# Performance work log

Hardware: AMD Instinct MI355X
Metric: run time of the kernel (lower is better)

## Reference

```python
import jax, jax.numpy as jnp
import numpy as np
import math

H, SQK, SV, PQK, PV = 12, 16, 16, 4, 8
C1, C2 = 384, 128
B, N = 1, 768


def _rand_rot(key, shape):
    # random proper rotation matrices via QR of gaussian matrices
    m = jax.random.normal(key, shape + (3, 3), dtype=jnp.float32)
    q, r = jnp.linalg.qr(m)
    d = jnp.sign(jnp.diagonal(r, axis1=-2, axis2=-1))
    return q * d[..., None, :]


def setup_inputs() -> dict:
    key = jax.random.key(0)
    ks = jax.random.split(key, 16)
    s = 0.05
    return {
        'act': jax.random.normal(ks[0], (B, N, C1), dtype=jnp.float32),
        'act_2d': jax.random.normal(ks[1], (B, N, N, C2), dtype=jnp.float32),
        'sequence_mask': jnp.ones((B, N, 1), dtype=jnp.float32),
        'rot': _rand_rot(ks[2], (B, N)),
        'trans': jax.random.normal(ks[3], (B, N, 3), dtype=jnp.float32),
        'wq': jax.random.normal(ks[4], (C1, H * SQK), dtype=jnp.float32) * s,
        'wk': jax.random.normal(ks[5], (C1, H * SQK), dtype=jnp.float32) * s,
        'wv': jax.random.normal(ks[6], (C1, H * SV), dtype=jnp.float32) * s,
        'wqp': jax.random.normal(ks[7], (C1, H * PQK * 3), dtype=jnp.float32) * s,
        'bqp': jnp.zeros((H * PQK * 3,), dtype=jnp.float32),
        'wkp': jax.random.normal(ks[8], (C1, H * PQK * 3), dtype=jnp.float32) * s,
        'bkp': jnp.zeros((H * PQK * 3,), dtype=jnp.float32),
        'wvp': jax.random.normal(ks[9], (C1, H * PV * 3), dtype=jnp.float32) * s,
        'bvp': jnp.zeros((H * PV * 3,), dtype=jnp.float32),
        'w2d': jax.random.normal(ks[10], (C2, H), dtype=jnp.float32) * s,
        'b2d': jnp.zeros((H,), dtype=jnp.float32),
        'wfin': jax.random.normal(ks[11], (H * (C2 + SV + 4 * PV), C1), dtype=jnp.float32) * s,
        'bfin': jnp.zeros((C1,), dtype=jnp.float32),
        'tw': jnp.zeros((H,), dtype=jnp.float32),
    }


def _points(act, w, b, P):
    # torch: view [...,H,P*3] -> split into 3 chunks of P -> stack last => layout [H,3,P]
    p = (act @ w + b).reshape(*act.shape[:-1], H, 3, P)
    p = jnp.moveaxis(p, -2, -1)  # [B,N,H,P,3]
    return p.reshape(*act.shape[:-1], H * P, 3)


def _ipa(act, act_2d, sequence_mask, rot, trans,
         wq, wk, wv, wqp, bqp, wkp, bkp, wvp, bvp, w2d, b2d, wfin, bfin, tw):
    b, n, _ = act.shape
    q = (act @ wq).reshape(b, n, H, SQK) * math.sqrt(1.0 / SQK)
    k = (act @ wk).reshape(b, n, H, SQK)
    v = (act @ wv).reshape(b, n, H, SV)

    apply = lambda p: jnp.einsum('bnij,bnpj->bnpi', rot, p) + trans[:, :, None, :]
    qp = apply(_points(act, wqp, bqp, PQK))  # [B,N,H*PQK,3]
    kp = apply(_points(act, wkp, bkp, PQK))
    vp = apply(_points(act, wvp, bvp, PV))   # [B,N,H*PV,3]

    # point-distance logits
    pw = math.sqrt(2.0 / (9.0 * PQK)) * jax.nn.softplus(tw)  # [H]
    d2 = jnp.sum(jnp.square(qp[:, :, None] - kp[:, None]), -1)  # [B,N,N,H*PQK]
    d2 = d2.reshape(b, n, n, H, PQK).sum(-1)                    # [B,N,N,H]
    logits = -0.5 * pw * d2
    logits = logits + jnp.einsum('bqhc,bkhc->bqkh', q, k)
    logits = logits + act_2d @ w2d + b2d
    mask_2d = sequence_mask * jnp.swapaxes(sequence_mask, -1, -2)  # [B,N,N]
    logits = logits - 1e5 * (1.0 - mask_2d)[..., None]
    logits = logits * math.sqrt(1.0 / 3.0)
    attn = jax.nn.softmax(logits, axis=-2)  # over key residues

    res_scalar = jnp.einsum('bqkh,bkhc->bqhc', attn, v).reshape(b, n, H * SV)
    vp5 = vp.reshape(b, n, H, PV, 3)
    rpg = jnp.einsum('bqkh,bkhpd->bqhpd', attn, vp5).reshape(b, n, H * PV, 3)
    rpl = jnp.einsum('bnji,bnpj->bnpi', rot, rpg - trans[:, :, None, :])  # invert_apply
    norms = jnp.linalg.norm(rpl, axis=-1)
    r2d = jnp.einsum('bijh,bijc->bihc', attn, act_2d).reshape(b, n, H * C2)
    final = jnp.concatenate(
        [res_scalar, rpl[..., 0], rpl[..., 1], rpl[..., 2], norms, r2d], axis=-1)
    return final @ wfin + bfin


def reference(act, act_2d, sequence_mask, rot, trans,
              wq, wk, wv, wqp, bqp, wkp, bkp, wvp, bvp, w2d, b2d, wfin, bfin, tw):
    return _ipa(act, act_2d, sequence_mask, rot, trans,
                wq, wk, wv, wqp, bqp, wkp, bkp, wvp, bvp, w2d, b2d, wfin, bfin, tw)
```

## Files before the change

### kernel.cpp

```cpp
#include <hip/hip_runtime.h>
#include <math.h>

#define NH    12
#define NRES  768
#define C1V   384
#define C2V   128
#define NPROJ 1152
#define QKD   28
#define FDIM  2112
#define VVD   480
#define APAD  772
#define KSPLIT 11

__device__ __forceinline__ float softplusf_(float x) {
    return (x > 20.f) ? x : log1pf(__expf(x));
}

__global__ __launch_bounds__(256) void k1_proj(
    const float* __restrict__ act,
    const float* __restrict__ wq, const float* __restrict__ wk,
    const float* __restrict__ wv, const float* __restrict__ wqp,
    const float* __restrict__ wkp, const float* __restrict__ wvp,
    const float* __restrict__ bqp, const float* __restrict__ bkp,
    const float* __restrict__ bvp, float* __restrict__ proj)
{
    __shared__ float As[64 * 33];
    __shared__ float Bs[32 * 65];
    const int n0 = blockIdx.x * 64, m0 = blockIdx.y * 64;
    const int tid = threadIdx.x;
    const int tx = tid & 15, ty = tid >> 4;
    float c[4][4] = {};

    for (int kt = 0; kt < C1V; kt += 32) {
        for (int idx = tid; idx < 64 * 32; idx += 256) {
            int r = idx >> 5, j = idx & 31;
            As[r * 33 + j] = act[(m0 + r) * C1V + kt + j];
        }
        for (int idx = tid; idx < 32 * 64; idx += 256) {
            int r = idx >> 6, col = idx & 63;
            int jj = n0 + col, k = kt + r;
            float w;
            if      (jj < 192) w = wq [k * 192 + jj];
            else if (jj < 384) w = wk [k * 192 + jj - 192];
            else if (jj < 576) w = wv [k * 192 + jj - 384];
            else if (jj < 720) w = wqp[k * 144 + jj - 576];
            else if (jj < 864) w = wkp[k * 144 + jj - 720];
            else               w = wvp[k * 288 + jj - 864];
            Bs[r * 65 + col] = w;
        }
        __syncthreads();
        #pragma unroll
        for (int kk = 0; kk < 32; ++kk) {
            float a[4], b[4];
            #pragma unroll
            for (int i = 0; i < 4; ++i) a[i] = As[(ty * 4 + i) * 33 + kk];
            #pragma unroll
            for (int j = 0; j < 4; ++j) b[j] = Bs[kk * 65 + tx * 4 + j];
            #pragma unroll
            for (int i = 0; i < 4; ++i)
                #pragma unroll
                for (int j = 0; j < 4; ++j) c[i][j] += a[i] * b[j];
        }
        __syncthreads();
    }
    float biasv[4];
    #pragma unroll
    for (int j = 0; j < 4; ++j) {
        int col = n0 + tx * 4 + j;
        biasv[j] = (col >= 864) ? bvp[col - 864]
                 : (col >= 720) ? bkp[col - 720]
                 : (col >= 576) ? bqp[col - 576] : 0.f;
    }
    #pragma unroll
    for (int i = 0; i < 4; ++i) {
        float4 v;
        v.x = c[i][0] + biasv[0]; v.y = c[i][1] + biasv[1];
        v.z = c[i][2] + biasv[2]; v.w = c[i][3] + biasv[3];
        *(float4*)&proj[(m0 + ty * 4 + i) * NPROJ + n0 + tx * 4] = v;
    }
}

__global__ __launch_bounds__(64) void k2_prep(
    const float* __restrict__ proj, const float* __restrict__ rot,
    const float* __restrict__ trans, const float* __restrict__ tw,
    float* __restrict__ Qv, float* __restrict__ Kv,
    float* __restrict__ akArr, float* __restrict__ vv)
{
    const int n = blockIdx.x, tid = threadIdx.x;
    __shared__ float kp2[48];
    const float* pr = proj + n * NPROJ;
    float R[9], T[3];
    #pragma unroll
    for (int i = 0; i < 9; ++i) R[i] = rot[n * 9 + i];
    #pragma unroll
    for (int i = 0; i < 3; ++i) T[i] = trans[n * 3 + i];

    for (int idx = tid; idx < 192; idx += 64) {
        int h = idx >> 4, cc = idx & 15;
        Qv[(n * NH + h) * QKD + cc] = pr[idx] * 0.25f;
        Kv[(n * NH + h) * QKD + cc] = pr[192 + idx];
        vv[n * VVD + idx] = pr[384 + idx];
    }
    if (tid < 48) {
        int h = tid >> 2, p = tid & 3;
        float pwh = 0.23570226039551584f * softplusf_(tw[h]);
        float lx = pr[576 + h * 12 + p];
        float ly = pr[576 + h * 12 + 4 + p];
        float lz = pr[576 + h * 12 + 8 + p];
        float gx = R[0] * lx + R[1] * ly + R[2] * lz + T[0];
        float gy = R[3] * lx + R[4] * ly + R[5] * lz + T[1];
        float gz = R[6] * lx + R[7] * ly + R[8] * lz + T[2];
        float* qd = &Qv[(n * NH + h) * QKD + 16];
        qd[p] = pwh * gx; qd[4 + p] = pwh * gy; qd[8 + p] = pwh * gz;
        lx = pr[720 + h * 12 + p];
        ly = pr[720 + h * 12 + 4 + p];
        lz = pr[720 + h * 12 + 8 + p];
        gx = R[0] * lx + R[1] * ly + R[2] * lz + T[0];
        gy = R[3] * lx + R[4] * ly + R[5] * lz + T[1];
        gz = R[6] * lx + R[7] * ly + R[8] * lz + T[2];
        float* kd = &Kv[(n * NH + h) * QKD + 16];
        kd[p] = gx; kd[4 + p] = gy; kd[8 + p] = gz;
        kp2[tid] = gx * gx + gy * gy + gz * gz;
    }
    __syncthreads();
    if (tid < NH) {
        float pwh = 0.23570226039551584f * softplusf_(tw[tid]);
        akArr[n * NH + tid] = -0.5f * pwh *
            (kp2[tid * 4] + kp2[tid * 4 + 1] + kp2[tid * 4 + 2] + kp2[tid * 4 + 3]);
    }
    for (int idx = tid; idx < 96; idx += 64) {
        int h = idx >> 3, p = idx & 7;
        float lx = pr[864 + h * 24 + p];
        float ly = pr[864 + h * 24 + 8 + p];
        float lz = pr[864 + h * 24 + 16 + p];
        float gx = R[0] * lx + R[1] * ly + R[2] * lz + T[0];
        float gy = R[3] * lx + R[4] * ly + R[5] * lz + T[1];
        float gz = R[6] * lx + R[7] * ly + R[8] * lz + T[2];
        float* dst = &vv[n * VVD + 192 + h * 24 + p * 3];
        dst[0] = gx; dst[1] = gy; dst[2] = gz;
    }
}

__global__ __launch_bounds__(256) void k2b_qk(
    const float* __restrict__ Qv, const float* __restrict__ Kv,
    const float* __restrict__ akArr, float* __restrict__ qkBuf)
{
    const int h = blockIdx.z;
    const int k0 = blockIdx.x * 64, q0 = blockIdx.y * 64;
    __shared__ float As[64 * 29];
    __shared__ float Bs[64 * 29];
    const int tid = threadIdx.x, tx = tid & 15, ty = tid >> 4;

    for (int idx = tid; idx < 64 * 28; idx += 256) {
        int r = idx / 28, j = idx - r * 28;
        As[r * 29 + j] = Qv[((q0 + r) * NH + h) * QKD + j];
        Bs[r * 29 + j] = Kv[((k0 + r) * NH + h) * QKD + j];
    }
    __syncthreads();
    float c[4][4] = {};
    #pragma unroll
    for (int kk = 0; kk < 28; ++kk) {
        float a[4], b[4];
        #pragma unroll
        for (int i = 0; i < 4; ++i) a[i] = As[(ty * 4 + i) * 29 + kk];
        #pragma unroll
        for (int j = 0; j < 4; ++j) b[j] = Bs[(tx * 4 + j) * 29 + kk];
        #pragma unroll
        for (int i = 0; i < 4; ++i)
            #pragma unroll
            for (int j = 0; j < 4; ++j) c[i][j] += a[i] * b[j];
    }
    float akv[4];
    #pragma unroll
    for (int j = 0; j < 4; ++j) akv[j] = akArr[(k0 + tx * 4 + j) * NH + h];
    #pragma unroll
    for (int i = 0; i < 4; ++i) {
        float4 v;
        v.x = c[i][0] + akv[0]; v.y = c[i][1] + akv[1];
        v.z = c[i][2] + akv[2]; v.w = c[i][3] + akv[3];
        *(float4*)&qkBuf[((q0 + ty * 4 + i) * NH + h) * NRES + k0 + tx * 4] = v;
    }
}

__global__ __launch_bounds__(256) void kA_bias(
    const float* __restrict__ act2d, const float* __restrict__ smask,
    const float* __restrict__ w2d, float* __restrict__ qkBuf)
{
    const int q = blockIdx.y, k0 = blockIdx.x * 64, tid = threadIdx.x;
    __shared__ float tile[64 * 129];
    __shared__ float w2dS[NH * 128];

    for (int idx = tid; idx < C2V * NH; idx += 256)
        w2dS[(idx % NH) * 128 + (idx / NH)] = w2d[idx];
    const float* src = act2d + ((size_t)q * NRES + k0) * C2V;
    #pragma unroll
    for (int i = 0; i < 8; ++i) {
        int f = tid + i * 256;
        float4 v = ((const float4*)src)[f];
        int r = f >> 5, cq = f & 31;
        float* dst = &tile[r * 129 + cq * 4];
        dst[0] = v.x; dst[1] = v.y; dst[2] = v.z; dst[3] = v.w;
    }
    __syncthreads();

    const int r = tid & 63, g = tid >> 6;
    const float* trow = &tile[r * 129];
    const float* w0 = &w2dS[(3 * g    ) * 128];
    const float* w1 = &w2dS[(3 * g + 1) * 128];
    const float* w2 = &w2dS[(3 * g + 2) * 128];
    float d0 = 0.f, d1 = 0.f, d2 = 0.f;
    #pragma unroll
    for (int c = 0; c < 128; ++c) {
        float t = trow[c];
        d0 += t * w0[c];
        d1 += t * w1[c];
        d2 += t * w2[c];
    }
    const int k = k0 + r;
    const float msk = -1e5f * (1.f - smask[q] * smask[k]);
    const float scale = 0.5773502691896258f;
    size_t i0 = ((size_t)(q * NH + 3 * g    )) * NRES + k;
    size_t i1 = ((size_t)(q * NH + 3 * g + 1)) * NRES + k;
    size_t i2 = ((size_t)(q * NH + 3 * g + 2)) * NRES + k;
    qkBuf[i0] = (qkBuf[i0] + d0 + msk) * scale;
    qkBuf[i1] = (qkBuf[i1] + d1 + msk) * scale;
    qkBuf[i2] = (qkBuf[i2] + d2 + msk) * scale;
}

__global__ __launch_bounds__(256) void kC_attn(
    const float* __restrict__ act2d, const float* __restrict__ qkBuf,
    const float* __restrict__ vv, const float* __restrict__ rot,
    const float* __restrict__ trans, float* __restrict__ F)
{
    const int q = blockIdx.x, tid = threadIdx.x;
    __shared__ float attnS[NH * APAD];
    __shared__ float tile[24 * 128];
    __shared__ float red[NH * 4];
    __shared__ float mh[NH], lh[NH];
    __shared__ float rotS[9], transS[3];

    if (tid < 9) rotS[tid] = rot[q * 9 + tid];
    if (tid < 3) transS[tid] = trans[q * 3 + tid];

    float lg[3][NH];
    #pragma unroll
    for (int h = 0; h < NH; ++h)
        #pragma unroll
        for (int i = 0; i < 3; ++i)
            lg[i][h] = qkBuf[((size_t)(q * NH + h)) * NRES + tid + 256 * i];

    const int wv_ = tid >> 6, lane = tid & 63;
    #pragma unroll
    for (int h = 0; h < NH; ++h) {
        float v = fmaxf(fmaxf(lg[0][h], lg[1][h]), lg[2][h]);
        for (int off = 32; off > 0; off >>= 1) v = fmaxf(v, __shfl_down(v, off, 64));
        if (lane == 0) red[h * 4 + wv_] = v;
    }
    __syncthreads();
    if (tid < NH)
        mh[tid] = fmaxf(fmaxf(red[tid * 4], red[tid * 4 + 1]),
                        fmaxf(red[tid * 4 + 2], red[tid * 4 + 3]));
    __syncthreads();
    float lsum[NH];
    #pragma unroll
    for (int h = 0; h < NH; ++h) lsum[h] = 0.f;
    #pragma unroll
    for (int i = 0; i < 3; ++i)
        #pragma unroll
        for (int h = 0; h < NH; ++h) {
            float e = __expf(lg[i][h] - mh[h]);
            attnS[h * APAD + tid + 256 * i] = e;
            lsum[h] += e;
        }
    #pragma unroll
    for (int h = 0; h < NH; ++h) {
        float v = lsum[h];
        for (int off = 32; off > 0; off >>= 1) v += __shfl_down(v, off, 64);
        if (lane == 0) red[h * 4 + wv_] = v;
    }
    __syncthreads();
    if (tid < NH)
        lh[tid] = 1.f / (red[tid * 4] + red[tid * 4 + 1] + red[tid * 4 + 2] + red[tid * 4 + 3]);

    const int c = tid & 127, kg = tid >> 7;
    float acc[NH];
    #pragma unroll
    for (int h = 0; h < NH; ++h) acc[h] = 0.f;

    for (int s = 0; s < 32; ++s) {
        const int k0 = s * 24;
        __syncthreads();
        const float* src = act2d + ((size_t)q * NRES + k0) * C2V;
        #pragma unroll
        for (int i = 0; i < 3; ++i) {
            int f = tid + i * 256;
            ((float4*)tile)[f] = ((const float4*)src)[f];
        }
        __syncthreads();
        #pragma unroll
        for (int k4 = 0; k4 < 3; ++k4) {
            const int kb = kg * 12 + k4 * 4;
            float4 av[NH];
            #pragma unroll
            for (int h = 0; h < NH; ++h)
                av[h] = *(const float4*)&attnS[h * APAD + k0 + kb];
            #pragma unroll
            for (int u = 0; u < 4; ++u) {
                float t = tile[(kb + u) * 128 + c];
                #pragma unroll
                for (int h = 0; h < NH; ++h)
                    acc[h] += ((const float*)&av[h])[u] * t;
            }
        }
    }
    __syncthreads();
    if (kg == 1) {
        #pragma unroll
        for (int h = 0; h < NH; ++h) tile[h * 128 + c] = acc[h];
    }
    __syncthreads();
    float* Fq = F + q * FDIM;
    if (kg == 0) {
        #pragma unroll
        for (int h = 0; h < NH; ++h)
            Fq[576 + h * 128 + c] = (acc[h] + tile[h * 128 + c]) * lh[h];
    }
    __syncthreads();

    const int j4 = tid & 127;
    const int kgv = tid >> 7;
    float p0 = 0.f, p1 = 0.f, p2 = 0.f, p3 = 0.f;
    if (j4 < 120) {
        const int h = (j4 < 48) ? (j4 >> 2) : ((j4 - 48) / 6);
        const float* at = &attnS[h * APAD + kgv * 384];
        const float* col = vv + (size_t)(kgv * 384) * VVD + j4 * 4;
        #pragma unroll 4
        for (int k = 0; k < 384; ++k) {
            float a = at[k];
            float4 v = *(const float4*)(col + (size_t)k * VVD);
            p0 += a * v.x; p1 += a * v.y; p2 += a * v.z; p3 += a * v.w;
        }
    }
    __syncthreads();
    if (j4 < 120) {
        float4 pv = {p0, p1, p2, p3};
        *(float4*)&tile[(kgv * 120 + j4) * 4] = pv;
    }
    __syncthreads();
    if (tid < 120) {
        float4 a = *(const float4*)&tile[tid * 4];
        float4 b = *(const float4*)&tile[(120 + tid) * 4];
        const int h = (tid < 48) ? (tid >> 2) : ((tid - 48) / 6);
        const float il = lh[h];
        float4 s = {(a.x + b.x) * il, (a.y + b.y) * il,
                    (a.z + b.z) * il, (a.w + b.w) * il};
        if (tid < 48) {
            *(float4*)&Fq[tid * 4] = s;
        } else {
            *(float4*)&tile[1024 + (tid - 48) * 4] = s;
        }
    }
    __syncthreads();
    if (tid < 96) {
        float gx = tile[1024 + tid * 3]     - transS[0];
        float gy = tile[1024 + tid * 3 + 1] - transS[1];
        float gz = tile[1024 + tid * 3 + 2] - transS[2];
        float x = rotS[0] * gx + rotS[3] * gy + rotS[6] * gz;
        float y = rotS[1] * gx + rotS[4] * gy + rotS[7] * gz;
        float z = rotS[2] * gx + rotS[5] * gy + rotS[8] * gz;
        Fq[192 + tid] = x;
        Fq[288 + tid] = y;
        Fq[384 + tid] = z;
        Fq[480 + tid] = sqrtf(x * x + y * y + z * z);
    }
}

__global__ __launch_bounds__(256) void k5_partial(
    const float* __restrict__ F, const float* __restrict__ wfin,
    float* __restrict__ part)
{
    const int n0 = blockIdx.x * 64, m0 = blockIdx.y * 64, kz = blockIdx.z;
    const int kbeg = kz * 192;
    __shared__ float As[64 * 33];
    __shared__ float Bs[32 * 65];
    const int tid = threadIdx.x, tx = tid & 15, ty = tid >> 4;
    float c[4][4] = {};

    for (int kt = kbeg; kt < kbeg + 192; kt += 32) {
        for (int idx = tid; idx < 64 * 32; idx += 256) {
            int r = idx >> 5, j = idx & 31;
            As[r * 33 + j] = F[(m0 + r) * FDIM + kt + j];
        }
        for (int idx = tid; idx < 32 * 64; idx += 256) {
            int r = idx >> 6, col = idx & 63;
            Bs[r * 65 + col] = wfin[(kt + r) * 384 + n0 + col];
        }
        __syncthreads();
        #pragma unroll
        for (int kk = 0; kk < 32; ++kk) {
            float a[4], b[4];
            #pragma unroll
            for (int i = 0; i < 4; ++i) a[i] = As[(ty * 4 + i) * 33 + kk];
            #pragma unroll
            for (int j = 0; j < 4; ++j) b[j] = Bs[kk * 65 + tx * 4 + j];
            #pragma unroll
            for (int i = 0; i < 4; ++i)
                #pragma unroll
                for (int j = 0; j < 4; ++j) c[i][j] += a[i] * b[j];
        }
        __syncthreads();
    }
    float* dst = part + (size_t)kz * (768 * 384);
    #pragma unroll
    for (int i = 0; i < 4; ++i) {
        float4 v = {c[i][0], c[i][1], c[i][2], c[i][3]};
        *(float4*)&dst[(m0 + ty * 4 + i) * 384 + n0 + tx * 4] = v;
    }
}

__global__ __launch_bounds__(256) void k5_reduce(
    const float* __restrict__ part, const float* __restrict__ bfin,
    float* __restrict__ out)
{
    const int e = blockIdx.x * 256 + threadIdx.x;
    const float4* p = (const float4*)part;
    float4 b = ((const float4*)bfin)[e % 96];
    float4 s = {b.x, b.y, b.z, b.w};
    #pragma unroll
    for (int kz = 0; kz < KSPLIT; ++kz) {
        float4 v = p[(size_t)kz * 73728 + e];
        s.x += v.x; s.y += v.y; s.z += v.z; s.w += v.w;
    }
    ((float4*)out)[e] = s;
}

extern "C" void kernel_launch(void* const* d_in, const int* in_sizes, int n_in,
                              void* d_out, int out_size, void* d_ws, size_t ws_size,
                              hipStream_t stream) {
    const float* act   = (const float*)d_in[0];
    const float* act2d = (const float*)d_in[1];
    const float* smask = (const float*)d_in[2];
    const float* rot   = (const float*)d_in[3];
    const float* trans = (const float*)d_in[4];
    const float* wq    = (const float*)d_in[5];
    const float* wk    = (const float*)d_in[6];
    const float* wvv   = (const float*)d_in[7];
    const float* wqp   = (const float*)d_in[8];
    const float* bqp   = (const float*)d_in[9];
    const float* wkp   = (const float*)d_in[10];
    const float* bkp   = (const float*)d_in[11];
    const float* wvp   = (const float*)d_in[12];
    const float* bvp   = (const float*)d_in[13];
    const float* w2d   = (const float*)d_in[14];
    const float* wfin  = (const float*)d_in[16];
    const float* bfin  = (const float*)d_in[17];
    const float* tw    = (const float*)d_in[18];

    float* W     = (float*)d_ws;
    float* proj  = W;
    float* Qv    = proj  + 768 * NPROJ;
    float* Kv    = Qv    + 768 * NH * QKD;
    float* akArr = Kv    + 768 * NH * QKD;
    float* vvA   = akArr + 768 * NH;
    float* qkBuf = vvA   + 768 * VVD;
    float* F     = qkBuf + 768 * NH * NRES;
    float* part  = qkBuf;

    k1_proj<<<dim3(18, 12), 256, 0, stream>>>(act, wq, wk, wvv, wqp, wkp, wvp,
                                              bqp, bkp, bvp, proj);
    k2_prep<<<dim3(NRES), 64, 0, stream>>>(proj, rot, trans, tw, Qv, Kv, akArr, vvA);
    k2b_qk<<<dim3(12, 12, NH), 256, 0, stream>>>(Qv, Kv, akArr, qkBuf);
    kA_bias<<<dim3(12, NRES), 256, 0, stream>>>(act2d, smask, w2d, qkBuf);
    kC_attn<<<dim3(NRES), 256, 0, stream>>>(act2d, qkBuf, vvA, rot, trans, F);
    k5_partial<<<dim3(6, 12, KSPLIT), 256, 0, stream>>>(F, wfin, part);
    k5_reduce<<<dim3(288), 256, 0, stream>>>(part, bfin, (float*)d_out);
}
```

Measured before the change: 708.7 us.

## Use bf16 MFMA for pair bias and restructure attention-weighted act_2d reduction

The pair-bias projection (act_2d @ w2d) now converts each 64x128 act_2d tile to bf16 and runs it through 16x16x32 bf16 MFMA, with a small prep kernel that transposes and converts w2d to bf16. The attention-weighted act_2d sum in the attention kernel drops its shared-memory staging and per-tile barriers. Each thread instead streams float4 rows of act_2d directly from global memory for three heads over half the keys. This cuts ALU work and LDS traffic on the two passes over the large act_2d tensor, at the cost of bf16 rounding in the logits bias and more redundant global reads across heads.

```diff
diff --git a/kernel.cpp b/kernel.cpp
--- a/kernel.cpp
+++ b/kernel.cpp
@@ -12,8 +12,24 @@
 #define APAD  772
 #define KSPLIT 11
 
+typedef __attribute__((ext_vector_type(8))) short bf16x8;
+typedef __attribute__((ext_vector_type(4))) float f32x4;
+
 __device__ __forceinline__ float softplusf_(float x) {
     return (x > 20.f) ? x : log1pf(__expf(x));
+}
+__device__ __forceinline__ ushort f2bf(float x) {
+    union { float f; unsigned u; } v; v.f = x;
+    unsigned r = (v.u + 0x7fffu + ((v.u >> 16) & 1u)) >> 16;
+    return (ushort)r;
+}
+
+__global__ __launch_bounds__(256) void kW_prep(
+    const float* __restrict__ w2d, ushort* __restrict__ w2dT)
+{
+    int idx = blockIdx.x * 256 + threadIdx.x;
+    int h = idx >> 7, c = idx & 127;
+    w2dT[idx] = (h < NH) ? f2bf(w2d[c * NH + h]) : (ushort)0;
 }
 
 __global__ __launch_bounds__(256) void k1_proj(
@@ -182,49 +198,52 @@
     }
 }
 
-__global__ __launch_bounds__(256) void kA_bias(
+__global__ __launch_bounds__(256) void kA_mfma(
     const float* __restrict__ act2d, const float* __restrict__ smask,
-    const float* __restrict__ w2d, float* __restrict__ qkBuf)
+    const ushort* __restrict__ w2dT, float* __restrict__ qkBuf)
 {
     const int q = blockIdx.y, k0 = blockIdx.x * 64, tid = threadIdx.x;
-    __shared__ float tile[64 * 129];
-    __shared__ float w2dS[NH * 128];
-
-    for (int idx = tid; idx < C2V * NH; idx += 256)
-        w2dS[(idx % NH) * 128 + (idx / NH)] = w2d[idx];
+    __shared__ ushort tile[64 * 136];
+    const int lane = tid & 63, wv = tid >> 6;
+    const int nb = lane & 15, quad = lane >> 4;
+
+    bf16x8 bfr[4];
+    #pragma unroll
+    for (int s = 0; s < 4; ++s)
+        bfr[s] = *(const bf16x8*)&w2dT[nb * 128 + quad * 8 + s * 32];
+
     const float* src = act2d + ((size_t)q * NRES + k0) * C2V;
     #pragma unroll
     for (int i = 0; i < 8; ++i) {
         int f = tid + i * 256;
+        int r = f >> 5, c4 = f & 31;
         float4 v = ((const float4*)src)[f];
-        int r = f >> 5, cq = f & 31;
-        float* dst = &tile[r * 129 + cq * 4];
-        dst[0] = v.x; dst[1] = v.y; dst[2] = v.z; dst[3] = v.w;
-    }
-    __syncthreads();
-
-    const int r = tid & 63, g = tid >> 6;
-    const float* trow = &tile[r * 129];
-    const float* w0 = &w2dS[(3 * g    ) * 128];
-    const float* w1 = &w2dS[(3 * g + 1) * 128];
-    const float* w2 = &w2dS[(3 * g + 2) * 128];
-    float d0 = 0.f, d1 = 0.f, d2 = 0.f;
-    #pragma unroll
-    for (int c = 0; c < 128; ++c) {
-        float t = trow[c];
-        d0 += t * w0[c];
-        d1 += t * w1[c];
-        d2 += t * w2[c];
-    }
-    const int k = k0 + r;
-    const float msk = -1e5f * (1.f - smask[q] * smask[k]);
-    const float scale = 0.5773502691896258f;
-    size_t i0 = ((size_t)(q * NH + 3 * g    )) * NRES + k;
-    size_t i1 = ((size_t)(q * NH + 3 * g + 1)) * NRES + k;
-    size_t i2 = ((size_t)(q * NH + 3 * g + 2)) * NRES + k;
-    qkBuf[i0] = (qkBuf[i0] + d0 + msk) * scale;
-    qkBuf[i1] = (qkBuf[i1] + d1 + msk) * scale;
-    qkBuf[i2] = (qkBuf[i2] + d2 + msk) * scale;
+        ushort4 o = { f2bf(v.x), f2bf(v.y), f2bf(v.z), f2bf(v.w) };
+        *(ushort4*)&tile[r * 136 + c4 * 4] = o;
+    }
+    __syncthreads();
+
+    f32x4 acc = {0.f, 0.f, 0.f, 0.f};
+    #pragma unroll
+    for (int s = 0; s < 4; ++s) {
+        bf16x8 af = *(const bf16x8*)&tile[(wv * 16 + nb) * 136 + quad * 8 + s * 32];
+        acc = __builtin_amdgcn_mfma_f32_16x16x32_bf16(af, bfr[s], acc, 0, 0, 0);
+    }
+
+    if (nb < NH) {
+        const int kb = k0 + wv * 16 + quad * 4;
+        float* dst = &qkBuf[((size_t)(q * NH + nb)) * NRES + kb];
+        float4 old = *(float4*)dst;
+        float4 sm = *(const float4*)&smask[kb];
+        const float smq = smask[q];
+        const float scale = 0.5773502691896258f;
+        float4 outv;
+        outv.x = (old.x + acc[0] - 1e5f * (1.f - smq * sm.x)) * scale;
+        outv.y = (old.y + acc[1] - 1e5f * (1.f - smq * sm.y)) * scale;
+        outv.z = (old.z + acc[2] - 1e5f * (1.f - smq * sm.z)) * scale;
+        outv.w = (old.w + acc[3] - 1e5f * (1.f - smq * sm.w)) * scale;
+        *(float4*)dst = outv;
+    }
 }
 
 __global__ __launch_bounds__(256) void kC_attn(
@@ -234,7 +253,7 @@
 {
     const int q = blockIdx.x, tid = threadIdx.x;
     __shared__ float attnS[NH * APAD];
-    __shared__ float tile[24 * 128];
+    __shared__ float scr[1536];
     __shared__ float red[NH * 4];
     __shared__ float mh[NH], lh[NH];
     __shared__ float rotS[9], transS[3];
@@ -281,49 +300,55 @@
     __syncthreads();
     if (tid < NH)
         lh[tid] = 1.f / (red[tid * 4] + red[tid * 4 + 1] + red[tid * 4 + 2] + red[tid * 4 + 3]);
-
-    const int c = tid & 127, kg = tid >> 7;
-    float acc[NH];
-    #pragma unroll
-    for (int h = 0; h < NH; ++h) acc[h] = 0.f;
-
-    for (int s = 0; s < 32; ++s) {
-        const int k0 = s * 24;
-        __syncthreads();
-        const float* src = act2d + ((size_t)q * NRES + k0) * C2V;
-        #pragma unroll
-        for (int i = 0; i < 3; ++i) {
-            int f = tid + i * 256;
-            ((float4*)tile)[f] = ((const float4*)src)[f];
-        }
-        __syncthreads();
-        #pragma unroll
-        for (int k4 = 0; k4 < 3; ++k4) {
-            const int kb = kg * 12 + k4 * 4;
-            float4 av[NH];
-            #pragma unroll
-            for (int h = 0; h < NH; ++h)
-                av[h] = *(const float4*)&attnS[h * APAD + k0 + kb];
-            #pragma unroll
-            for (int u = 0; u < 4; ++u) {
-                float t = tile[(kb + u) * 128 + c];
-                #pragma unroll
-                for (int h = 0; h < NH; ++h)
-                    acc[h] += ((const float*)&av[h])[u] * t;
-            }
-        }
-    }
-    __syncthreads();
+    __syncthreads();
+
+    const int cq = tid & 31, hg = (tid >> 5) & 3, kg = tid >> 7;
+    const int h0 = 3 * hg;
+    const float* abase = act2d + ((size_t)q * NRES + kg * 384) * C2V + cq * 4;
+    const float* at0 = &attnS[(h0    ) * APAD + kg * 384];
+    const float* at1 = &attnS[(h0 + 1) * APAD + kg * 384];
+    const float* at2 = &attnS[(h0 + 2) * APAD + kg * 384];
+    float4 a0 = {0,0,0,0}, a1 = {0,0,0,0}, a2 = {0,0,0,0};
+
+    for (int kk = 0; kk < 384; kk += 4) {
+        float4 t0 = *(const float4*)&abase[(size_t)(kk    ) * C2V];
+        float4 t1 = *(const float4*)&abase[(size_t)(kk + 1) * C2V];
+        float4 t2 = *(const float4*)&abase[(size_t)(kk + 2) * C2V];
+        float4 t3 = *(const float4*)&abase[(size_t)(kk + 3) * C2V];
+        float4 p0 = *(const float4*)&at0[kk];
+        float4 p1 = *(const float4*)&at1[kk];
+        float4 p2 = *(const float4*)&at2[kk];
+        a0.x += p0.x*t0.x + p0.y*t1.x + p0.z*t2.x + p0.w*t3.x;
+        a0.y += p0.x*t0.y + p0.y*t1.y + p0.z*t2.y + p0.w*t3.y;
+        a0.z += p0.x*t0.z + p0.y*t1.z + p0.z*t2.z + p0.w*t3.z;
+        a0.w += p0.x*t0.w + p0.y*t1.w + p0.z*t2.w + p0.w*t3.w;
+        a1.x += p1.x*t0.x + p1.y*t1.x + p1.z*t2.x + p1.w*t3.x;
+        a1.y += p1.x*t0.y + p1.y*t1.y + p1.z*t2.y + p1.w*t3.y;
+        a1.z += p1.x*t0.z + p1.y*t1.z + p1.z*t2.z + p1.w*t3.z;
+        a1.w += p1.x*t0.w + p1.y*t1.w + p1.z*t2.w + p1.w*t3.w;
+        a2.x += p2.x*t0.x + p2.y*t1.x + p2.z*t2.x + p2.w*t3.x;
+        a2.y += p2.x*t0.y + p2.y*t1.y + p2.z*t2.y + p2.w*t3.y;
+        a2.z += p2.x*t0.z + p2.y*t1.z + p2.z*t2.z + p2.w*t3.z;
+        a2.w += p2.x*t0.w + p2.y*t1.w + p2.z*t2.w + p2.w*t3.w;
+    }
     if (kg == 1) {
-        #pragma unroll
-        for (int h = 0; h < NH; ++h) tile[h * 128 + c] = acc[h];
+        *(float4*)&scr[(h0    ) * 128 + cq * 4] = a0;
+        *(float4*)&scr[(h0 + 1) * 128 + cq * 4] = a1;
+        *(float4*)&scr[(h0 + 2) * 128 + cq * 4] = a2;
     }
     __syncthreads();
     float* Fq = F + q * FDIM;
     if (kg == 0) {
-        #pragma unroll
-        for (int h = 0; h < NH; ++h)
-            Fq[576 + h * 128 + c] = (acc[h] + tile[h * 128 + c]) * lh[h];
+        float4 b0 = *(const float4*)&scr[(h0    ) * 128 + cq * 4];
+        float4 b1 = *(const float4*)&scr[(h0 + 1) * 128 + cq * 4];
+        float4 b2 = *(const float4*)&scr[(h0 + 2) * 128 + cq * 4];
+        float l0 = lh[h0], l1 = lh[h0 + 1], l2 = lh[h0 + 2];
+        float4 o0 = {(a0.x+b0.x)*l0, (a0.y+b0.y)*l0, (a0.z+b0.z)*l0, (a0.w+b0.w)*l0};
+        float4 o1 = {(a1.x+b1.x)*l1, (a1.y+b1.y)*l1, (a1.z+b1.z)*l1, (a1.w+b1.w)*l1};
+        float4 o2 = {(a2.x+b2.x)*l2, (a2.y+b2.y)*l2, (a2.z+b2.z)*l2, (a2.w+b2.w)*l2};
+        *(float4*)&Fq[576 + (h0    ) * 128 + cq * 4] = o0;
+        *(float4*)&Fq[576 + (h0 + 1) * 128 + cq * 4] = o1;
+        *(float4*)&Fq[576 + (h0 + 2) * 128 + cq * 4] = o2;
     }
     __syncthreads();
 
@@ -344,12 +369,12 @@
     __syncthreads();
     if (j4 < 120) {
         float4 pv = {p0, p1, p2, p3};
-        *(float4*)&tile[(kgv * 120 + j4) * 4] = pv;
+        *(float4*)&scr[(kgv * 120 + j4) * 4] = pv;
     }
     __syncthreads();
     if (tid < 120) {
-        float4 a = *(const float4*)&tile[tid * 4];
-        float4 b = *(const float4*)&tile[(120 + tid) * 4];
+        float4 a = *(const float4*)&scr[tid * 4];
+        float4 b = *(const float4*)&scr[(120 + tid) * 4];
         const int h = (tid < 48) ? (tid >> 2) : ((tid - 48) / 6);
         const float il = lh[h];
         float4 s = {(a.x + b.x) * il, (a.y + b.y) * il,
@@ -357,14 +382,14 @@
         if (tid < 48) {
             *(float4*)&Fq[tid * 4] = s;
         } else {
-            *(float4*)&tile[1024 + (tid - 48) * 4] = s;
+            *(float4*)&scr[1024 + (tid - 48) * 4] = s;
         }
     }
     __syncthreads();
     if (tid < 96) {
-        float gx = tile[1024 + tid * 3]     - transS[0];
-        float gy = tile[1024 + tid * 3 + 1] - transS[1];
-        float gz = tile[1024 + tid * 3 + 2] - transS[2];
+        float gx = scr[1024 + tid * 3]     - transS[0];
+        float gy = scr[1024 + tid * 3 + 1] - transS[1];
+        float gz = scr[1024 + tid * 3 + 2] - transS[2];
         float x = rotS[0] * gx + rotS[3] * gy + rotS[6] * gz;
         float y = rotS[1] * gx + rotS[4] * gy + rotS[7] * gz;
         float z = rotS[2] * gx + rotS[5] * gy + rotS[8] * gz;
@@ -464,13 +489,15 @@
     float* vvA   = akArr + 768 * NH;
     float* qkBuf = vvA   + 768 * VVD;
     float* F     = qkBuf + 768 * NH * NRES;
+    ushort* w2dT = (ushort*)(F + 768 * FDIM);
     float* part  = qkBuf;
 
+    kW_prep<<<dim3(8), 256, 0, stream>>>(w2d, w2dT);
     k1_proj<<<dim3(18, 12), 256, 0, stream>>>(act, wq, wk, wvv, wqp, wkp, wvp,
                                               bqp, bkp, bvp, proj);
     k2_prep<<<dim3(NRES), 64, 0, stream>>>(proj, rot, trans, tw, Qv, Kv, akArr, vvA);
     k2b_qk<<<dim3(12, 12, NH), 256, 0, stream>>>(Qv, Kv, akArr, qkBuf);
-    kA_bias<<<dim3(12, NRES), 256, 0, stream>>>(act2d, smask, w2d, qkBuf);
+    kA_mfma<<<dim3(12, NRES), 256, 0, stream>>>(act2d, smask, w2dT, qkBuf);
     kC_attn<<<dim3(NRES), 256, 0, stream>>>(act2d, qkBuf, vvA, rot, trans, F);
     k5_partial<<<dim3(6, 12, KSPLIT), 256, 0, stream>>>(F, wfin, part);
     k5_reduce<<<dim3(288), 256, 0, stream>>>(part, bfin, (float*)d_out);
```

Result: faster. 686.8 us (-3.1%).
